# Kernel tuning notes

Hardware: AMD Instinct MI355X
Metric: run time of the kernel (lower is better)

Reference implementation:

```python
import jax, jax.numpy as jnp
import numpy as np
import math

B, T, C, H, RANK, RD = 8, 512, 2048, 16, 8, 16
HD = C // H  # 128
ADAPTER_SCALE = 1.0 / RANK  # scale / rank with scale=1.0


def setup_inputs() -> dict:
    key = jax.random.key(0)
    ks = jax.random.split(key, 7)
    x = jax.random.normal(ks[0], (B, T, C), dtype=jnp.float32)
    # frozen random linears (weights ~ N(0,1)/sqrt(in_features))
    Wqkv = jax.random.normal(ks[1], (3 * C, C), dtype=jnp.float32) / math.sqrt(C)
    Wout = jax.random.normal(ks[2], (C, C), dtype=jnp.float32) / math.sqrt(C)
    # VeRA frozen random matrices
    A0_qkv = jax.random.normal(ks[3], (RANK, C), dtype=jnp.float32) / math.sqrt(C)
    B0_qkv = jax.random.normal(ks[4], (3 * C, RANK), dtype=jnp.float32) / math.sqrt(RANK)
    A0_out = jax.random.normal(ks[5], (RANK, C), dtype=jnp.float32) / math.sqrt(C)
    B0_out = jax.random.normal(ks[6], (C, RANK), dtype=jnp.float32) / math.sqrt(RANK)
    # learned scaling vectors (init to ones, as in the module)
    d_a_qkv = jnp.ones((RANK,), dtype=jnp.float32)
    d_b_qkv = jnp.ones((RANK,), dtype=jnp.float32)
    d_a_out = jnp.ones((RANK,), dtype=jnp.float32)
    d_b_out = jnp.ones((RANK,), dtype=jnp.float32)
    # partial RoPE caches over first RD dims
    freqs = 1.0 / (10000.0 ** (jnp.arange(0, RD, 2, dtype=jnp.float32) / RD))  # [RD/2]
    ang = jnp.arange(T, dtype=jnp.float32)[:, None] * freqs[None, :]  # [T, RD/2]
    cos = jnp.cos(ang)
    sin = jnp.sin(ang)
    return {"x": x, "Wqkv": Wqkv, "A0_qkv": A0_qkv, "B0_qkv": B0_qkv,
            "d_a_qkv": d_a_qkv, "d_b_qkv": d_b_qkv,
            "Wout": Wout, "A0_out": A0_out, "B0_out": B0_out,
            "d_a_out": d_a_out, "d_b_out": d_b_out,
            "cos": cos, "sin": sin}


def _adapted_linear(x, W, A0, B0, d_a, d_b):
    # frozen(x) + VeRA adapter: diag(d_b) B0 diag(d_a) A0, scaled by 1/rank
    base = x @ W.T
    h = (x @ A0.T) * (d_a * d_b)
    return base + (h @ B0.T) * ADAPTER_SCALE


def _apply_rope(q, cos, sin):
    # q: [B, H, T, HD]; rotate first RD dims, pass-through the rest
    x_rope, x_pass = q[..., :RD], q[..., RD:]
    half = RD // 2
    x1, x2 = x_rope[..., :half], x_rope[..., half:]
    c = cos[None, None]  # [1,1,T,RD/2]
    s = sin[None, None]
    rot = jnp.concatenate([x1 * c - x2 * s, x2 * c + x1 * s], axis=-1)
    return jnp.concatenate([rot, x_pass], axis=-1)


def reference(x, Wqkv, A0_qkv, B0_qkv, d_a_qkv, d_b_qkv,
              Wout, A0_out, B0_out, d_a_out, d_b_out, cos, sin):
    qkv = _adapted_linear(x, Wqkv, A0_qkv, B0_qkv, d_a_qkv, d_b_qkv)  # [B,T,3C]
    qkv = qkv.reshape(B, T, 3, H, HD)
    q = jnp.transpose(qkv[:, :, 0], (0, 2, 1, 3))  # [B,H,T,HD]
    k = jnp.transpose(qkv[:, :, 1], (0, 2, 1, 3))
    v = jnp.transpose(qkv[:, :, 2], (0, 2, 1, 3))
    q = _apply_rope(q, cos, sin)
    k = _apply_rope(k, cos, sin)
    # causal SDPA
    scale = 1.0 / math.sqrt(HD)
    scores = jnp.einsum('bhqd,bhkd->bhqk', q, k) * scale
    mask = jnp.tril(jnp.ones((T, T), dtype=bool))
    scores = jnp.where(mask[None, None], scores, jnp.finfo(scores.dtype).min)
    attn = jax.nn.softmax(scores, axis=-1)
    y = jnp.einsum('bhqk,bhkd->bhqd', attn, v)  # [B,H,T,HD]
    y = jnp.transpose(y, (0, 2, 1, 3)).reshape(B, T, C)
    return _adapted_linear(y, Wout, A0_out, B0_out, d_a_out, d_b_out)
```

## Files before the change

kernel.cpp:

```cpp
#include <hip/hip_runtime.h>

typedef unsigned short ushort_t;
typedef __attribute__((ext_vector_type(8))) short short8;
typedef __attribute__((ext_vector_type(4))) float f32x4;

#define AS1(p) ((const __attribute__((address_space(1))) void*)(p))
#define AS3(p) ((__attribute__((address_space(3))) void*)(p))

__device__ __forceinline__ ushort_t f2bf(float f){
  unsigned u = __float_as_uint(f);
  u += 0x7FFFu + ((u>>16)&1u);
  return (ushort_t)(u>>16);
}
__device__ __forceinline__ float bf2f(ushort_t h){
  return __uint_as_float(((unsigned)h)<<16);
}

__global__ __launch_bounds__(256) void conv_f2b(const float* __restrict__ src,
                                                ushort_t* __restrict__ dst, int n){
  int i = (blockIdx.x*256 + threadIdx.x)*4;
  if (i < n){
    float4 v = *(const float4*)&src[i];
    ushort_t o0=f2bf(v.x), o1=f2bf(v.y), o2=f2bf(v.z), o3=f2bf(v.w);
    ushort4 o; o.x=o0; o.y=o1; o.z=o2; o.w=o3;
    *(ushort4*)&dst[i] = o;
  }
}

__global__ __launch_bounds__(256) void lora_h_f32(const float* __restrict__ X,
                                                  ushort_t* __restrict__ Xbf,
                                                  const float* __restrict__ A0,
                                                  const float* __restrict__ da,
                                                  const float* __restrict__ db,
                                                  float* __restrict__ out, int K){
  int m = blockIdx.x;
  int tid = threadIdx.x, lane = tid & 63, w = tid >> 6;
  float part[8] = {0,0,0,0,0,0,0,0};
  for (int k = tid; k < K; k += 256){
    float xv = X[(size_t)m*K + k];
    Xbf[(size_t)m*K + k] = f2bf(xv);
    #pragma unroll
    for (int r=0;r<8;++r) part[r] += xv * A0[r*K + k];
  }
  #pragma unroll
  for (int r=0;r<8;++r)
    for (int d=1;d<64;d<<=1) part[r] += __shfl_xor(part[r], d, 64);
  __shared__ float wsum[4][8];
  if (lane==0){
    #pragma unroll
    for (int r=0;r<8;++r) wsum[w][r] = part[r];
  }
  __syncthreads();
  if (tid < 8){
    float s = wsum[0][tid]+wsum[1][tid]+wsum[2][tid]+wsum[3][tid];
    out[(size_t)m*8 + tid] = s * da[tid]*db[tid];
  }
}

__global__ __launch_bounds__(256) void lora_h_bf16(const ushort_t* __restrict__ X,
                                                   const float* __restrict__ A0,
                                                   const float* __restrict__ da,
                                                   const float* __restrict__ db,
                                                   float* __restrict__ out, int K){
  int m = blockIdx.x;
  int tid = threadIdx.x, lane = tid & 63, w = tid >> 6;
  float part[8] = {0,0,0,0,0,0,0,0};
  for (int k = tid; k < K; k += 256){
    float xv = bf2f(X[(size_t)m*K + k]);
    #pragma unroll
    for (int r=0;r<8;++r) part[r] += xv * A0[r*K + k];
  }
  #pragma unroll
  for (int r=0;r<8;++r)
    for (int d=1;d<64;d<<=1) part[r] += __shfl_xor(part[r], d, 64);
  __shared__ float wsum[4][8];
  if (lane==0){
    #pragma unroll
    for (int r=0;r<8;++r) wsum[w][r] = part[r];
  }
  __syncthreads();
  if (tid < 8){
    float s = wsum[0][tid]+wsum[1][tid]+wsum[2][tid]+wsum[3][tid];
    out[(size_t)m*8 + tid] = s * da[tid]*db[tid];
  }
}

__global__ __launch_bounds__(512, 1) void gemm256_lora(
    const ushort_t* __restrict__ A, const ushort_t* __restrict__ Bw,
    const float* __restrict__ hmat, const float* __restrict__ B0,
    ushort_t* __restrict__ C, int M, int N, int K)
{
  __shared__ __align__(16) char smem[131072];
  const int tid = threadIdx.x, lane = tid & 63, w = tid >> 6;
  const int wm = w >> 2, wn = w & 3;

  const int nbn = N >> 8;
  const int nwg = (M >> 8) * nbn;
  const int q8 = nwg >> 3;
  const int swz = ((int)blockIdx.x & 7)*q8 + ((int)blockIdx.x >> 3);
  const int m0 = (swz / nbn) << 8, n0 = (swz % nbn) << 8;

  const int NTt = K >> 6;
  const int srow   = tid >> 3;
  const int schunk = (lane & 7) ^ (lane >> 3);

  #define STAGE_A(h, tt, bb) do { \
    const ushort_t* g_ = A + (size_t)(m0 + (h)*128 + srow)*K + (tt)*64 + schunk*8; \
    __builtin_amdgcn_global_load_lds(AS1(g_), AS3(smem + (bb)*32768 + (h)*16384 + tid*16), 16, 0, 0); \
    __builtin_amdgcn_global_load_lds(AS1(g_ + (size_t)64*K), AS3(smem + (bb)*32768 + (h)*16384 + 8192 + tid*16), 16, 0, 0); \
  } while(0)
  #define STAGE_B(h, tt, bb) do { \
    const ushort_t* g_ = Bw + (size_t)(n0 + (h)*128 + srow)*K + (tt)*64 + schunk*8; \
    __builtin_amdgcn_global_load_lds(AS1(g_), AS3(smem + 65536 + (bb)*32768 + (h)*16384 + tid*16), 16, 0, 0); \
    __builtin_amdgcn_global_load_lds(AS1(g_ + (size_t)64*K), AS3(smem + 65536 + (bb)*32768 + (h)*16384 + 8192 + tid*16), 16, 0, 0); \
  } while(0)

  #define RDA(bb, q, kk) (*(const short8*)(smem + (bb)*32768 + ((q)>>2)*16384 + \
      (((q)&3)*32 + wm*16 + (lane&15))*128 + ((((kk)*4 + (lane>>4)) ^ (lane&7))<<4)))
  #define RDB(bb, r, kk) (*(const short8*)(smem + 65536 + (bb)*32768 + ((r)>>1)*16384 + \
      (((r)&1)*64 + wn*16 + (lane&15))*128 + ((((kk)*4 + (lane>>4)) ^ (lane&7))<<4)))

  #define MM(q, ai, r, bi) do{ \
    acc[q][r] = __builtin_amdgcn_mfma_f32_16x16x32_bf16(aF[ai][0], bF[bi][0], acc[q][r], 0,0,0); \
    acc[q][r] = __builtin_amdgcn_mfma_f32_16x16x32_bf16(aF[ai][1], bF[bi][1], acc[q][r], 0,0,0); \
  }while(0)

  #define BARRIER() asm volatile("s_barrier" ::: "memory")
  #define LGKM0()  do{ asm volatile("s_waitcnt lgkmcnt(0)" ::: "memory"); __builtin_amdgcn_sched_barrier(0); }while(0)

  short8 aF[4][2];
  short8 bF[2][2];
  f32x4 acc[8][4] = {};

  STAGE_A(0,0,0); STAGE_B(0,0,0); STAGE_A(1,0,0); STAGE_B(1,0,0);
  asm volatile("s_waitcnt vmcnt(4)" ::: "memory");
  BARRIER();

  for (int t = 0; t < NTt-1; ++t){
    const int b = t & 1, nb = b ^ 1;
    #pragma unroll
    for (int q=0;q<4;++q){ aF[q][0]=RDA(b,q,0); aF[q][1]=RDA(b,q,1); }
    #pragma unroll
    for (int rl=0;rl<2;++rl){ bF[rl][0]=RDB(b,rl,0); bF[rl][1]=RDB(b,rl,1); }
    STAGE_A(0, t+1, nb);
    BARRIER(); LGKM0();
    __builtin_amdgcn_s_setprio(1);
    MM(0,0,0,0); MM(0,0,1,1); MM(1,1,0,0); MM(1,1,1,1);
    MM(2,2,0,0); MM(2,2,1,1); MM(3,3,0,0); MM(3,3,1,1);
    __builtin_amdgcn_s_setprio(0);
    asm volatile("s_waitcnt vmcnt(4)" ::: "memory");
    BARRIER();
    #pragma unroll
    for (int q=0;q<4;++q){ aF[q][0]=RDA(b,q+4,0); aF[q][1]=RDA(b,q+4,1); }
    STAGE_B(0, t+1, nb);
    BARRIER(); LGKM0();
    __builtin_amdgcn_s_setprio(1);
    MM(4,0,0,0); MM(4,0,1,1); MM(5,1,0,0); MM(5,1,1,1);
    MM(6,2,0,0); MM(6,2,1,1); MM(7,3,0,0); MM(7,3,1,1);
    __builtin_amdgcn_s_setprio(0);
    asm volatile("s_waitcnt vmcnt(4)" ::: "memory");
    BARRIER();
    #pragma unroll
    for (int q=0;q<4;++q){ aF[q][0]=RDA(b,q,0); aF[q][1]=RDA(b,q,1); }
    #pragma unroll
    for (int rl=0;rl<2;++rl){ bF[rl][0]=RDB(b,rl+2,0); bF[rl][1]=RDB(b,rl+2,1); }
    STAGE_A(1, t+1, nb);
    BARRIER(); LGKM0();
    __builtin_amdgcn_s_setprio(1);
    MM(0,0,2,0); MM(0,0,3,1); MM(1,1,2,0); MM(1,1,3,1);
    MM(2,2,2,0); MM(2,2,3,1); MM(3,3,2,0); MM(3,3,3,1);
    __builtin_amdgcn_s_setprio(0);
    BARRIER();
    #pragma unroll
    for (int q=0;q<4;++q){ aF[q][0]=RDA(b,q+4,0); aF[q][1]=RDA(b,q+4,1); }
    STAGE_B(1, t+1, nb);
    BARRIER(); LGKM0();
    __builtin_amdgcn_s_setprio(1);
    MM(4,0,2,0); MM(4,0,3,1); MM(5,1,2,0); MM(5,1,3,1);
    MM(6,2,2,0); MM(6,2,3,1); MM(7,3,2,0); MM(7,3,3,1);
    __builtin_amdgcn_s_setprio(0);
    asm volatile("s_waitcnt vmcnt(4)" ::: "memory");
    BARRIER();
  }

  {
    const int b = (NTt-1) & 1;
    #pragma unroll
    for (int q=0;q<4;++q){ aF[q][0]=RDA(b,q,0); aF[q][1]=RDA(b,q,1); }
    #pragma unroll
    for (int rl=0;rl<2;++rl){ bF[rl][0]=RDB(b,rl,0); bF[rl][1]=RDB(b,rl,1); }
    BARRIER(); LGKM0();
    __builtin_amdgcn_s_setprio(1);
    MM(0,0,0,0); MM(0,0,1,1); MM(1,1,0,0); MM(1,1,1,1);
    MM(2,2,0,0); MM(2,2,1,1); MM(3,3,0,0); MM(3,3,1,1);
    __builtin_amdgcn_s_setprio(0);
    asm volatile("s_waitcnt vmcnt(2)" ::: "memory");
    BARRIER();
    #pragma unroll
    for (int q=0;q<4;++q){ aF[q][0]=RDA(b,q+4,0); aF[q][1]=RDA(b,q+4,1); }
    BARRIER(); LGKM0();
    __builtin_amdgcn_s_setprio(1);
    MM(4,0,0,0); MM(4,0,1,1); MM(5,1,0,0); MM(5,1,1,1);
    MM(6,2,0,0); MM(6,2,1,1); MM(7,3,0,0); MM(7,3,1,1);
    __builtin_amdgcn_s_setprio(0);
    asm volatile("s_waitcnt vmcnt(0)" ::: "memory");
    BARRIER();
    #pragma unroll
    for (int q=0;q<4;++q){ aF[q][0]=RDA(b,q,0); aF[q][1]=RDA(b,q,1); }
    #pragma unroll
    for (int rl=0;rl<2;++rl){ bF[rl][0]=RDB(b,rl+2,0); bF[rl][1]=RDB(b,rl+2,1); }
    LGKM0();
    MM(0,0,2,0); MM(0,0,3,1); MM(1,1,2,0); MM(1,1,3,1);
    MM(2,2,2,0); MM(2,2,3,1); MM(3,3,2,0); MM(3,3,3,1);
    BARRIER();
    #pragma unroll
    for (int q=0;q<4;++q){ aF[q][0]=RDA(b,q+4,0); aF[q][1]=RDA(b,q+4,1); }
    LGKM0();
    MM(4,0,2,0); MM(4,0,3,1); MM(5,1,2,0); MM(5,1,3,1);
    MM(6,2,2,0); MM(6,2,3,1); MM(7,3,2,0); MM(7,3,3,1);
  }

  float b0v[4][8];
  #pragma unroll
  for (int r=0;r<4;++r){
    int col = n0 + r*64 + wn*16 + (lane&15);
    const float4* bp = (const float4*)&B0[(size_t)col*8];
    float4 u0 = bp[0], u1 = bp[1];
    b0v[r][0]=u0.x; b0v[r][1]=u0.y; b0v[r][2]=u0.z; b0v[r][3]=u0.w;
    b0v[r][4]=u1.x; b0v[r][5]=u1.y; b0v[r][6]=u1.z; b0v[r][7]=u1.w;
  }
  #pragma unroll
  for (int q=0;q<8;++q){
    #pragma unroll
    for (int jj=0;jj<4;++jj){
      int row = m0 + q*32 + wm*16 + (lane>>4)*4 + jj;
      const float4* hp = (const float4*)&hmat[(size_t)row*8];
      float4 h0 = hp[0], h1 = hp[1];
      #pragma unroll
      for (int r=0;r<4;++r){
        float lor = h0.x*b0v[r][0]+h0.y*b0v[r][1]+h0.z*b0v[r][2]+h0.w*b0v[r][3]
                  + h1.x*b0v[r][4]+h1.y*b0v[r][5]+h1.z*b0v[r][6]+h1.w*b0v[r][7];
        int col = n0 + r*64 + wn*16 + (lane&15);
        C[(size_t)row*N + col] = f2bf(acc[q][r][jj] + 0.125f*lor);
      }
    }
  }
  #undef STAGE_A
  #undef STAGE_B
  #undef RDA
  #undef RDB
  #undef MM
  #undef BARRIER
  #undef LGKM0
}

template<int MODE>
__global__ __launch_bounds__(512, 1) void gemm128x256_lora(
    const ushort_t* __restrict__ A, const ushort_t* __restrict__ Bw,
    const float* __restrict__ hmat, const float* __restrict__ B0,
    void* __restrict__ C, int M, int N, int K)
{
  __shared__ __align__(16) char smem[98304];
  const int tid = threadIdx.x, lane = tid & 63, w = tid >> 6;
  const int wm = w >> 2, wn = w & 3;

  const int nbn = N >> 8;
  const int nwg = (M >> 7) * nbn;
  const int q8 = nwg >> 3;
  const int swz = ((int)blockIdx.x & 7)*q8 + ((int)blockIdx.x >> 3);
  const int m0 = (swz / nbn) << 7, n0 = (swz % nbn) << 8;

  const int NTt = K >> 6;

  const int srow8  = tid >> 3;
  const int schunk = (lane & 7) ^ (lane >> 3);

  #define STAGE_AU(u, tt, bb) do { \
    const ushort_t* g_ = A + (size_t)(m0 + (u)*64 + srow8)*K + (tt)*64 + schunk*8; \
    __builtin_amdgcn_global_load_lds(AS1(g_), AS3(smem + (bb)*16384 + (u)*8192 + w*1024), 16, 0, 0); \
  } while(0)
  #define STAGE_BU(u, tt, bb) do { \
    const ushort_t* g_ = Bw + (size_t)(n0 + (u)*64 + srow8)*K + (tt)*64 + schunk*8; \
    __builtin_amdgcn_global_load_lds(AS1(g_), AS3(smem + 32768 + (bb)*32768 + (u)*8192 + w*1024), 16, 0, 0); \
  } while(0)

  #define RDA(bb, q, kk) (*(const short8*)(smem + (bb)*16384 + \
      ((q)*32 + wm*16 + (lane&15))*128 + ((((kk)*4 + (lane>>4)) ^ (lane&7))<<4)))
  #define RDB(bb, rg, kk) (*(const short8*)(smem + 32768 + (bb)*32768 + \
      ((rg)*64 + wn*16 + (lane&15))*128 + ((((kk)*4 + (lane>>4)) ^ (lane&7))<<4)))

  #define MM0(q,rl) do{ \
    acc[q][rl] = __builtin_amdgcn_mfma_f32_16x16x32_bf16(aF[q][0], bF[rl][0], acc[q][rl], 0,0,0); \
    acc[q][rl] = __builtin_amdgcn_mfma_f32_16x16x32_bf16(aF[q][1], bF[rl][1], acc[q][rl], 0,0,0); \
  }while(0)
  #define MM1(q,rl) do{ \
    acc[q][(rl)+2] = __builtin_amdgcn_mfma_f32_16x16x32_bf16(aF[q][0], bF[rl][0], acc[q][(rl)+2], 0,0,0); \
    acc[q][(rl)+2] = __builtin_amdgcn_mfma_f32_16x16x32_bf16(aF[q][1], bF[rl][1], acc[q][(rl)+2], 0,0,0); \
  }while(0)

  #define BARRIER() asm volatile("s_barrier" ::: "memory")

  short8 aF[4][2];
  short8 bF[2][2];
  f32x4 acc[4][4] = {};

  STAGE_AU(0,0,0); STAGE_AU(1,0,0); STAGE_BU(0,0,0); STAGE_BU(1,0,0);
  STAGE_BU(2,0,0); STAGE_BU(3,0,0);
  asm volatile("s_waitcnt vmcnt(2)" ::: "memory");
  BARRIER();

  for (int t = 0; t < NTt-1; ++t){
    const int b = t & 1, nb = b ^ 1;
    #pragma unroll
    for (int q=0;q<4;++q){ aF[q][0]=RDA(b,q,0); aF[q][1]=RDA(b,q,1); }
    #pragma unroll
    for (int rl=0;rl<2;++rl){ bF[rl][0]=RDB(b,rl,0); bF[rl][1]=RDB(b,rl,1); }
    STAGE_AU(0,t+1,nb); STAGE_AU(1,t+1,nb); STAGE_BU(0,t+1,nb); STAGE_BU(1,t+1,nb);
    __builtin_amdgcn_s_setprio(1);
    MM0(0,0); MM0(0,1); MM0(1,0); MM0(1,1);
    MM0(2,0); MM0(2,1); MM0(3,0); MM0(3,1);
    __builtin_amdgcn_s_setprio(0);
    asm volatile("s_waitcnt vmcnt(4)" ::: "memory");
    BARRIER();
    #pragma unroll
    for (int rl=0;rl<2;++rl){ bF[rl][0]=RDB(b,rl+2,0); bF[rl][1]=RDB(b,rl+2,1); }
    STAGE_BU(2,t+1,nb); STAGE_BU(3,t+1,nb);
    __builtin_amdgcn_s_setprio(1);
    MM1(0,0); MM1(0,1); MM1(1,0); MM1(1,1);
    MM1(2,0); MM1(2,1); MM1(3,0); MM1(3,1);
    __builtin_amdgcn_s_setprio(0);
    asm volatile("s_waitcnt lgkmcnt(0)" ::: "memory");
    asm volatile("s_waitcnt vmcnt(2)" ::: "memory");
    BARRIER();
  }

  {
    const int b = (NTt-1) & 1;
    #pragma unroll
    for (int q=0;q<4;++q){ aF[q][0]=RDA(b,q,0); aF[q][1]=RDA(b,q,1); }
    #pragma unroll
    for (int rl=0;rl<2;++rl){ bF[rl][0]=RDB(b,rl,0); bF[rl][1]=RDB(b,rl,1); }
    __builtin_amdgcn_s_setprio(1);
    MM0(0,0); MM0(0,1); MM0(1,0); MM0(1,1);
    MM0(2,0); MM0(2,1); MM0(3,0); MM0(3,1);
    __builtin_amdgcn_s_setprio(0);
    asm volatile("s_waitcnt vmcnt(0)" ::: "memory");
    BARRIER();
    #pragma unroll
    for (int rl=0;rl<2;++rl){ bF[rl][0]=RDB(b,rl+2,0); bF[rl][1]=RDB(b,rl+2,1); }
    MM1(0,0); MM1(0,1); MM1(1,0); MM1(1,1);
    MM1(2,0); MM1(2,1); MM1(3,0); MM1(3,1);
  }

  float b0v[4][8];
  #pragma unroll
  for (int r=0;r<4;++r){
    int col = n0 + r*64 + wn*16 + (lane&15);
    const float4* bp = (const float4*)&B0[(size_t)col*8];
    float4 u0 = bp[0], u1 = bp[1];
    b0v[r][0]=u0.x; b0v[r][1]=u0.y; b0v[r][2]=u0.z; b0v[r][3]=u0.w;
    b0v[r][4]=u1.x; b0v[r][5]=u1.y; b0v[r][6]=u1.z; b0v[r][7]=u1.w;
  }
  #pragma unroll
  for (int q=0;q<4;++q){
    #pragma unroll
    for (int jj=0;jj<4;++jj){
      int row = m0 + q*32 + wm*16 + (lane>>4)*4 + jj;
      const float4* hp = (const float4*)&hmat[(size_t)row*8];
      float4 h0 = hp[0], h1 = hp[1];
      #pragma unroll
      for (int r=0;r<4;++r){
        float lor = h0.x*b0v[r][0]+h0.y*b0v[r][1]+h0.z*b0v[r][2]+h0.w*b0v[r][3]
                  + h1.x*b0v[r][4]+h1.y*b0v[r][5]+h1.z*b0v[r][6]+h1.w*b0v[r][7];
        int col = n0 + r*64 + wn*16 + (lane&15);
        float v = acc[q][r][jj] + 0.125f*lor;
        if (MODE==0) ((ushort_t*)C)[(size_t)row*N + col] = f2bf(v);
        else         ((float*)C)[(size_t)row*N + col]    = v;
      }
    }
  }
  #undef STAGE_AU
  #undef STAGE_BU
  #undef RDA
  #undef RDB
  #undef MM0
  #undef MM1
  #undef BARRIER
}

__global__ __launch_bounds__(256) void rope_kernel(ushort_t* __restrict__ qkv,
                                                   const float* __restrict__ cosb,
                                                   const float* __restrict__ sinb){
  int idx = blockIdx.x*256 + threadIdx.x;
  int d = idx & 7;
  int g = idx >> 3;
  int h_ = g & 15;
  int s  = (g>>4) & 1;
  int t  = (g>>5) & 511;
  int b  = g >> 14;
  size_t base = (size_t)(b*512 + t)*6144 + s*2048 + h_*128;
  float x1 = bf2f(qkv[base+d]), x2 = bf2f(qkv[base+d+8]);
  float c = cosb[t*8+d], sn = sinb[t*8+d];
  qkv[base+d]   = f2bf(x1*c - x2*sn);
  qkv[base+d+8] = f2bf(x2*c + x1*sn);
}

__global__ __launch_bounds__(256) void attn_kernel(const ushort_t* __restrict__ qkv,
                                                   ushort_t* __restrict__ y){
  __shared__ __align__(16) ushort_t Ks[64*128];
  __shared__ __align__(16) ushort_t Vt[128*64];
  __shared__ __align__(16) ushort_t Pl[4][16*64];

  const int qt = blockIdx.x, hh = blockIdx.y, b = blockIdx.z;
  const int tid = threadIdx.x, lane = tid & 63, w = tid >> 6, g = lane >> 4;
  const int qb0 = qt*64;
  const int row_base = b*512;
  const int qoff = hh*128;
  const int koff = 2048 + hh*128;
  const int voff = 4096 + hh*128;
  const float scale = 0.08838834764831845f;

  short8 qf[4];
  {
    int qr = qb0 + w*16 + (lane & 15);
    const ushort_t* qp = qkv + (size_t)(row_base + qr)*6144 + qoff + g*8;
    #pragma unroll
    for (int kc=0;kc<4;++kc) qf[kc] = *(const short8*)(qp + kc*32);
  }

  const int krow = tid >> 4;
  const int kc_  = tid & 15;
  const int kcs  = (kc_ & 8) | ((kc_ ^ (krow & 7)) & 7);
  const int vr   = tid >> 2;
  const int vd0  = (tid & 3) * 32;
  const int vrhi = vr >> 3, vrlo = vr & 7;

  f32x4 o[8] = {};
  float mrow[4] = {-1e30f,-1e30f,-1e30f,-1e30f};
  float lrow[4] = {0,0,0,0};

  for (int t = 0; t <= qt; ++t){
    const int kv0 = t*64;
    __syncthreads();
    {
      const ushort_t* kg = qkv + (size_t)(row_base + kv0 + krow)*6144 + koff + kcs*8;
      #pragma unroll
      for (int i=0;i<4;++i)
        __builtin_amdgcn_global_load_lds(AS1(kg + (size_t)(i*16)*6144),
                                         AS3((char*)Ks + i*4096 + tid*16), 16, 0, 0);
    }
    {
      const ushort_t* vg = qkv + (size_t)(row_base + kv0 + vr)*6144 + voff + vd0;
      short8 vv0 = ((const short8*)vg)[0];
      short8 vv1 = ((const short8*)vg)[1];
      short8 vv2 = ((const short8*)vg)[2];
      short8 vv3 = ((const short8*)vg)[3];
      #pragma unroll
      for (int ii=0;ii<8;++ii){
        int sw = (vrhi ^ ii) << 3;
        Vt[(vd0 + ii     )*64 + sw + vrlo] = (ushort_t)vv0[ii];
        Vt[(vd0 + 8 + ii )*64 + sw + vrlo] = (ushort_t)vv1[ii];
        Vt[(vd0 + 16 + ii)*64 + sw + vrlo] = (ushort_t)vv2[ii];
        Vt[(vd0 + 24 + ii)*64 + sw + vrlo] = (ushort_t)vv3[ii];
      }
    }
    __syncthreads();

    f32x4 s4[4] = {};
    #pragma unroll
    for (int cg=0;cg<4;++cg){
      const int row = cg*16 + (lane&15);
      const int rx = row & 7;
      #pragma unroll
      for (int kc=0;kc<4;++kc){
        const int ch = kc*4 + g;
        const short8 kfv = *(const short8*)&Ks[row*128 + (((ch&8)|((ch^rx)&7))<<3)];
        s4[cg] = __builtin_amdgcn_mfma_f32_16x16x32_bf16(qf[kc], kfv, s4[cg], 0, 0, 0);
      }
    }

    const bool diag = (t == qt);
    float fac[4], p0[4], p1[4], p2[4], p3[4];
    #pragma unroll
    for (int j=0;j<4;++j){
      float a0 = s4[0][j]*scale, a1 = s4[1][j]*scale, a2 = s4[2][j]*scale, a3 = s4[3][j]*scale;
      if (diag){
        int q_abs = qb0 + w*16 + g*4 + j;
        int c0 = kv0 + (lane&15);
        if (c0      > q_abs) a0 = -1e30f;
        if (c0 + 16 > q_abs) a1 = -1e30f;
        if (c0 + 32 > q_abs) a2 = -1e30f;
        if (c0 + 48 > q_abs) a3 = -1e30f;
      }
      float mx = fmaxf(fmaxf(a0,a1), fmaxf(a2,a3));
      #pragma unroll
      for (int d=1; d<16; d<<=1) mx = fmaxf(mx, __shfl_xor(mx, d, 16));
      float mn = fmaxf(mrow[j], mx);
      float f  = __expf(mrow[j] - mn);
      mrow[j] = mn; fac[j] = f;
      p0[j] = __expf(a0 - mn); p1[j] = __expf(a1 - mn);
      p2[j] = __expf(a2 - mn); p3[j] = __expf(a3 - mn);
      float rs = p0[j] + p1[j] + p2[j] + p3[j];
      #pragma unroll
      for (int d=1; d<16; d<<=1) rs += __shfl_xor(rs, d, 16);
      lrow[j] = lrow[j]*f + rs;
    }
    #pragma unroll
    for (int n=0;n<8;++n){
      #pragma unroll
      for (int j=0;j<4;++j) o[n][j] *= fac[j];
    }

    {
      ushort_t* plw = &Pl[w][0];
      #pragma unroll
      for (int j=0;j<4;++j){
        const int prow = g*4 + j;
        const int rx = prow & 7;
        const int cl = (lane&15)>>3, c7 = lane&7;
        plw[prow*64 + (((0*2+cl)^rx)<<3) + c7] = f2bf(p0[j]);
        plw[prow*64 + (((1*2+cl)^rx)<<3) + c7] = f2bf(p1[j]);
        plw[prow*64 + (((2*2+cl)^rx)<<3) + c7] = f2bf(p2[j]);
        plw[prow*64 + (((3*2+cl)^rx)<<3) + c7] = f2bf(p3[j]);
      }
    }
    {
      const ushort_t* plw = &Pl[w][0];
      const int rowP = lane & 15, rxp = rowP & 7;
      const short8 pf0 = *(const short8*)&plw[rowP*64 + (((g  )^rxp)<<3)];
      const short8 pf1 = *(const short8*)&plw[rowP*64 + (((4+g)^rxp)<<3)];
      #pragma unroll
      for (int n=0;n<8;++n){
        const int d = n*16 + (lane&15);
        const int dx = d & 7;
        const short8 vf0 = *(const short8*)&Vt[d*64 + (((g  )^dx)<<3)];
        const short8 vf1 = *(const short8*)&Vt[d*64 + (((4+g)^dx)<<3)];
        o[n] = __builtin_amdgcn_mfma_f32_16x16x32_bf16(pf0, vf0, o[n], 0, 0, 0);
        o[n] = __builtin_amdgcn_mfma_f32_16x16x32_bf16(pf1, vf1, o[n], 0, 0, 0);
      }
    }
  }

  #pragma unroll
  for (int j=0;j<4;++j){
    float inv = 1.0f / lrow[j];
    int qr = qb0 + w*16 + g*4 + j;
    #pragma unroll
    for (int n=0;n<8;++n)
      y[(size_t)(row_base+qr)*2048 + hh*128 + n*16 + (lane&15)] = f2bf(o[n][j]*inv);
  }
}

extern "C" void kernel_launch(void* const* d_in, const int* in_sizes, int n_in,
                              void* d_out, int out_size, void* d_ws, size_t ws_size,
                              hipStream_t stream){
  const float* x       = (const float*)d_in[0];
  const float* Wqkv    = (const float*)d_in[1];
  const float* A0_qkv  = (const float*)d_in[2];
  const float* B0_qkv  = (const float*)d_in[3];
  const float* da_qkv  = (const float*)d_in[4];
  const float* db_qkv  = (const float*)d_in[5];
  const float* Wout    = (const float*)d_in[6];
  const float* A0_out  = (const float*)d_in[7];
  const float* B0_out  = (const float*)d_in[8];
  const float* da_out  = (const float*)d_in[9];
  const float* db_out  = (const float*)d_in[10];
  const float* cosb    = (const float*)d_in[11];
  const float* sinb    = (const float*)d_in[12];
  float* out = (float*)d_out;

  char* ws = (char*)d_ws;
  ushort_t* x_bf    = (ushort_t*)(ws);
  ushort_t* wqkv_bf = (ushort_t*)(ws + 16777216);
  ushort_t* wout_bf = (ushort_t*)(ws + 41943040);
  ushort_t* qkv_bf  = (ushort_t*)(ws + 50331648);
  ushort_t* y_bf    = (ushort_t*)(ws + 100663296);
  float*    h_qkv   = (float*)   (ws + 117440512);
  float*    h_out   = (float*)   (ws + 117571584);

  const int M = 4096;
  const int C = 2048;
  const int N3 = 6144;

  conv_f2b<<<12288,256, 0, stream>>>(Wqkv, wqkv_bf, N3*C);
  conv_f2b<<<4096, 256, 0, stream>>>(Wout, wout_bf, C*C);

  lora_h_f32<<<M, 256, 0, stream>>>(x, x_bf, A0_qkv, da_qkv, db_qkv, h_qkv, C);

  gemm256_lora<<<(M/256)*(N3/256), 512, 0, stream>>>(x_bf, wqkv_bf, h_qkv, B0_qkv,
                                                     qkv_bf, M, N3, C);

  rope_kernel<<<4096, 256, 0, stream>>>(qkv_bf, cosb, sinb);

  attn_kernel<<<dim3(8, 16, 8), 256, 0, stream>>>(qkv_bf, y_bf);

  lora_h_bf16<<<M, 256, 0, stream>>>(y_bf, A0_out, da_out, db_out, h_out, C);

  gemm128x256_lora<1><<<(M/128)*(C/256), 512, 0, stream>>>(y_bf, wout_bf, h_out, B0_out,
                                                           out, M, C, C);
}
```

Measured before the change: 272.5 us.

## Retile QKV GEMM to 256x192 blocks with reworked 3-phase pipeline

Changes the QKV projection GEMM tile from 256x256 to 256x192. The grid grows from 384 to 512 workgroups, which gives a whole number of waves on a 256-CU device instead of a partial second wave. The 8 waves are regrouped as 4x2, each owning a 64x96 sub-tile. The K-loop is restructured into three MFMA phases per k-step, with the next tile's loads interleaved and fewer barriers and lgkm waits. The trade-off is less operand reuse per tile and a more delicate hand-written vmcnt/barrier schedule.

New measurement: 251.5 us. 7.7% less time.

```diff
diff --git a/kernel.cpp b/kernel.cpp
--- a/kernel.cpp
+++ b/kernel.cpp
@@ -85,55 +85,53 @@
   }
 }
 
-__global__ __launch_bounds__(512, 1) void gemm256_lora(
+__global__ __launch_bounds__(512, 1) void gemm256x192_lora(
     const ushort_t* __restrict__ A, const ushort_t* __restrict__ Bw,
     const float* __restrict__ hmat, const float* __restrict__ B0,
     ushort_t* __restrict__ C, int M, int N, int K)
 {
-  __shared__ __align__(16) char smem[131072];
+  __shared__ __align__(16) char smem[114688];
   const int tid = threadIdx.x, lane = tid & 63, w = tid >> 6;
-  const int wm = w >> 2, wn = w & 3;
-
-  const int nbn = N >> 8;
+  const int wm = w >> 1, wn = w & 1;
+
+  const int nbn = N / 192;
   const int nwg = (M >> 8) * nbn;
   const int q8 = nwg >> 3;
   const int swz = ((int)blockIdx.x & 7)*q8 + ((int)blockIdx.x >> 3);
-  const int m0 = (swz / nbn) << 8, n0 = (swz % nbn) << 8;
+  const int m0 = (swz / nbn) << 8, n0 = (swz % nbn) * 192;
 
   const int NTt = K >> 6;
-  const int srow   = tid >> 3;
+  const int srow8  = tid >> 3;
   const int schunk = (lane & 7) ^ (lane >> 3);
 
-  #define STAGE_A(h, tt, bb) do { \
-    const ushort_t* g_ = A + (size_t)(m0 + (h)*128 + srow)*K + (tt)*64 + schunk*8; \
-    __builtin_amdgcn_global_load_lds(AS1(g_), AS3(smem + (bb)*32768 + (h)*16384 + tid*16), 16, 0, 0); \
-    __builtin_amdgcn_global_load_lds(AS1(g_ + (size_t)64*K), AS3(smem + (bb)*32768 + (h)*16384 + 8192 + tid*16), 16, 0, 0); \
+  #define STAGE_AU(u, tt, bb) do { \
+    const ushort_t* g_ = A + (size_t)(m0 + (u)*64 + srow8)*K + (tt)*64 + schunk*8; \
+    __builtin_amdgcn_global_load_lds(AS1(g_), AS3(smem + (bb)*32768 + (u)*8192 + tid*16), 16, 0, 0); \
   } while(0)
-  #define STAGE_B(h, tt, bb) do { \
-    const ushort_t* g_ = Bw + (size_t)(n0 + (h)*128 + srow)*K + (tt)*64 + schunk*8; \
-    __builtin_amdgcn_global_load_lds(AS1(g_), AS3(smem + 65536 + (bb)*32768 + (h)*16384 + tid*16), 16, 0, 0); \
-    __builtin_amdgcn_global_load_lds(AS1(g_ + (size_t)64*K), AS3(smem + 65536 + (bb)*32768 + (h)*16384 + 8192 + tid*16), 16, 0, 0); \
+  #define STAGE_BU(u, tt, bb) do { \
+    const ushort_t* g_ = Bw + (size_t)(n0 + (u)*64 + srow8)*K + (tt)*64 + schunk*8; \
+    __builtin_amdgcn_global_load_lds(AS1(g_), AS3(smem + 65536 + (bb)*24576 + (u)*8192 + tid*16), 16, 0, 0); \
   } while(0)
 
-  #define RDA(bb, q, kk) (*(const short8*)(smem + (bb)*32768 + ((q)>>2)*16384 + \
-      (((q)&3)*32 + wm*16 + (lane&15))*128 + ((((kk)*4 + (lane>>4)) ^ (lane&7))<<4)))
-  #define RDB(bb, r, kk) (*(const short8*)(smem + 65536 + (bb)*32768 + ((r)>>1)*16384 + \
-      (((r)&1)*64 + wn*16 + (lane&15))*128 + ((((kk)*4 + (lane>>4)) ^ (lane&7))<<4)))
-
-  #define MM(q, ai, r, bi) do{ \
-    acc[q][r] = __builtin_amdgcn_mfma_f32_16x16x32_bf16(aF[ai][0], bF[bi][0], acc[q][r], 0,0,0); \
-    acc[q][r] = __builtin_amdgcn_mfma_f32_16x16x32_bf16(aF[ai][1], bF[bi][1], acc[q][r], 0,0,0); \
+  #define RDA(bb, q, kk) (*(const short8*)(smem + (bb)*32768 + \
+      ((q)*64 + wm*16 + (lane&15))*128 + ((((kk)*4 + (lane>>4)) ^ (lane&7))<<4)))
+  #define RDB(bb, r, kk) (*(const short8*)(smem + 65536 + (bb)*24576 + \
+      ((r)*32 + wn*16 + (lane&15))*128 + ((((kk)*4 + (lane>>4)) ^ (lane&7))<<4)))
+
+  #define MM(q, r, bi) do{ \
+    acc[q][r] = __builtin_amdgcn_mfma_f32_16x16x32_bf16(aF[q][0], bF[bi][0], acc[q][r], 0,0,0); \
+    acc[q][r] = __builtin_amdgcn_mfma_f32_16x16x32_bf16(aF[q][1], bF[bi][1], acc[q][r], 0,0,0); \
   }while(0)
 
   #define BARRIER() asm volatile("s_barrier" ::: "memory")
-  #define LGKM0()  do{ asm volatile("s_waitcnt lgkmcnt(0)" ::: "memory"); __builtin_amdgcn_sched_barrier(0); }while(0)
 
   short8 aF[4][2];
   short8 bF[2][2];
-  f32x4 acc[8][4] = {};
-
-  STAGE_A(0,0,0); STAGE_B(0,0,0); STAGE_A(1,0,0); STAGE_B(1,0,0);
-  asm volatile("s_waitcnt vmcnt(4)" ::: "memory");
+  f32x4 acc[4][6] = {};
+
+  STAGE_AU(0,0,0); STAGE_AU(1,0,0); STAGE_AU(2,0,0); STAGE_AU(3,0,0);
+  STAGE_BU(0,0,0); STAGE_BU(1,0,0); STAGE_BU(2,0,0);
+  asm volatile("s_waitcnt vmcnt(2)" ::: "memory");
   BARRIER();
 
   for (int t = 0; t < NTt-1; ++t){
@@ -142,44 +140,31 @@
     for (int q=0;q<4;++q){ aF[q][0]=RDA(b,q,0); aF[q][1]=RDA(b,q,1); }
     #pragma unroll
     for (int rl=0;rl<2;++rl){ bF[rl][0]=RDB(b,rl,0); bF[rl][1]=RDB(b,rl,1); }
-    STAGE_A(0, t+1, nb);
-    BARRIER(); LGKM0();
-    __builtin_amdgcn_s_setprio(1);
-    MM(0,0,0,0); MM(0,0,1,1); MM(1,1,0,0); MM(1,1,1,1);
-    MM(2,2,0,0); MM(2,2,1,1); MM(3,3,0,0); MM(3,3,1,1);
-    __builtin_amdgcn_s_setprio(0);
-    asm volatile("s_waitcnt vmcnt(4)" ::: "memory");
-    BARRIER();
-    #pragma unroll
-    for (int q=0;q<4;++q){ aF[q][0]=RDA(b,q+4,0); aF[q][1]=RDA(b,q+4,1); }
-    STAGE_B(0, t+1, nb);
-    BARRIER(); LGKM0();
-    __builtin_amdgcn_s_setprio(1);
-    MM(4,0,0,0); MM(4,0,1,1); MM(5,1,0,0); MM(5,1,1,1);
-    MM(6,2,0,0); MM(6,2,1,1); MM(7,3,0,0); MM(7,3,1,1);
-    __builtin_amdgcn_s_setprio(0);
-    asm volatile("s_waitcnt vmcnt(4)" ::: "memory");
-    BARRIER();
-    #pragma unroll
-    for (int q=0;q<4;++q){ aF[q][0]=RDA(b,q,0); aF[q][1]=RDA(b,q,1); }
+    STAGE_AU(0,t+1,nb); STAGE_AU(1,t+1,nb);
+    __builtin_amdgcn_s_setprio(1);
+    MM(0,0,0); MM(0,1,1); MM(1,0,0); MM(1,1,1);
+    MM(2,0,0); MM(2,1,1); MM(3,0,0); MM(3,1,1);
+    __builtin_amdgcn_s_setprio(0);
+    asm volatile("s_waitcnt vmcnt(3)" ::: "memory");
+    BARRIER();
     #pragma unroll
     for (int rl=0;rl<2;++rl){ bF[rl][0]=RDB(b,rl+2,0); bF[rl][1]=RDB(b,rl+2,1); }
-    STAGE_A(1, t+1, nb);
-    BARRIER(); LGKM0();
-    __builtin_amdgcn_s_setprio(1);
-    MM(0,0,2,0); MM(0,0,3,1); MM(1,1,2,0); MM(1,1,3,1);
-    MM(2,2,2,0); MM(2,2,3,1); MM(3,3,2,0); MM(3,3,3,1);
-    __builtin_amdgcn_s_setprio(0);
-    BARRIER();
-    #pragma unroll
-    for (int q=0;q<4;++q){ aF[q][0]=RDA(b,q+4,0); aF[q][1]=RDA(b,q+4,1); }
-    STAGE_B(1, t+1, nb);
-    BARRIER(); LGKM0();
-    __builtin_amdgcn_s_setprio(1);
-    MM(4,0,2,0); MM(4,0,3,1); MM(5,1,2,0); MM(5,1,3,1);
-    MM(6,2,2,0); MM(6,2,3,1); MM(7,3,2,0); MM(7,3,3,1);
-    __builtin_amdgcn_s_setprio(0);
-    asm volatile("s_waitcnt vmcnt(4)" ::: "memory");
+    STAGE_AU(2,t+1,nb); STAGE_AU(3,t+1,nb); STAGE_BU(0,t+1,nb);
+    __builtin_amdgcn_s_setprio(1);
+    MM(0,2,0); MM(0,3,1); MM(1,2,0); MM(1,3,1);
+    MM(2,2,0); MM(2,3,1); MM(3,2,0); MM(3,3,1);
+    __builtin_amdgcn_s_setprio(0);
+    asm volatile("s_waitcnt vmcnt(5)" ::: "memory");
+    BARRIER();
+    #pragma unroll
+    for (int rl=0;rl<2;++rl){ bF[rl][0]=RDB(b,rl+4,0); bF[rl][1]=RDB(b,rl+4,1); }
+    STAGE_BU(1,t+1,nb); STAGE_BU(2,t+1,nb);
+    __builtin_amdgcn_s_setprio(1);
+    MM(0,4,0); MM(0,5,1); MM(1,4,0); MM(1,5,1);
+    MM(2,4,0); MM(2,5,1); MM(3,4,0); MM(3,5,1);
+    __builtin_amdgcn_s_setprio(0);
+    asm volatile("s_waitcnt lgkmcnt(0)" ::: "memory");
+    asm volatile("s_waitcnt vmcnt(2)" ::: "memory");
     BARRIER();
   }
 
@@ -189,69 +174,57 @@
     for (int q=0;q<4;++q){ aF[q][0]=RDA(b,q,0); aF[q][1]=RDA(b,q,1); }
     #pragma unroll
     for (int rl=0;rl<2;++rl){ bF[rl][0]=RDB(b,rl,0); bF[rl][1]=RDB(b,rl,1); }
-    BARRIER(); LGKM0();
-    __builtin_amdgcn_s_setprio(1);
-    MM(0,0,0,0); MM(0,0,1,1); MM(1,1,0,0); MM(1,1,1,1);
-    MM(2,2,0,0); MM(2,2,1,1); MM(3,3,0,0); MM(3,3,1,1);
-    __builtin_amdgcn_s_setprio(0);
-    asm volatile("s_waitcnt vmcnt(2)" ::: "memory");
-    BARRIER();
-    #pragma unroll
-    for (int q=0;q<4;++q){ aF[q][0]=RDA(b,q+4,0); aF[q][1]=RDA(b,q+4,1); }
-    BARRIER(); LGKM0();
-    __builtin_amdgcn_s_setprio(1);
-    MM(4,0,0,0); MM(4,0,1,1); MM(5,1,0,0); MM(5,1,1,1);
-    MM(6,2,0,0); MM(6,2,1,1); MM(7,3,0,0); MM(7,3,1,1);
+    __builtin_amdgcn_s_setprio(1);
+    MM(0,0,0); MM(0,1,1); MM(1,0,0); MM(1,1,1);
+    MM(2,0,0); MM(2,1,1); MM(3,0,0); MM(3,1,1);
+    __builtin_amdgcn_s_setprio(0);
+    asm volatile("s_waitcnt vmcnt(1)" ::: "memory");
+    BARRIER();
+    #pragma unroll
+    for (int rl=0;rl<2;++rl){ bF[rl][0]=RDB(b,rl+2,0); bF[rl][1]=RDB(b,rl+2,1); }
+    __builtin_amdgcn_s_setprio(1);
+    MM(0,2,0); MM(0,3,1); MM(1,2,0); MM(1,3,1);
+    MM(2,2,0); MM(2,3,1); MM(3,2,0); MM(3,3,1);
     __builtin_amdgcn_s_setprio(0);
     asm volatile("s_waitcnt vmcnt(0)" ::: "memory");
     BARRIER();
     #pragma unroll
-    for (int q=0;q<4;++q){ aF[q][0]=RDA(b,q,0); aF[q][1]=RDA(b,q,1); }
-    #pragma unroll
-    for (int rl=0;rl<2;++rl){ bF[rl][0]=RDB(b,rl+2,0); bF[rl][1]=RDB(b,rl+2,1); }
-    LGKM0();
-    MM(0,0,2,0); MM(0,0,3,1); MM(1,1,2,0); MM(1,1,3,1);
-    MM(2,2,2,0); MM(2,2,3,1); MM(3,3,2,0); MM(3,3,3,1);
-    BARRIER();
-    #pragma unroll
-    for (int q=0;q<4;++q){ aF[q][0]=RDA(b,q+4,0); aF[q][1]=RDA(b,q+4,1); }
-    LGKM0();
-    MM(4,0,2,0); MM(4,0,3,1); MM(5,1,2,0); MM(5,1,3,1);
-    MM(6,2,2,0); MM(6,2,3,1); MM(7,3,2,0); MM(7,3,3,1);
-  }
-
-  float b0v[4][8];
-  #pragma unroll
-  for (int r=0;r<4;++r){
-    int col = n0 + r*64 + wn*16 + (lane&15);
+    for (int rl=0;rl<2;++rl){ bF[rl][0]=RDB(b,rl+4,0); bF[rl][1]=RDB(b,rl+4,1); }
+    MM(0,4,0); MM(0,5,1); MM(1,4,0); MM(1,5,1);
+    MM(2,4,0); MM(2,5,1); MM(3,4,0); MM(3,5,1);
+  }
+
+  float b0v[6][8];
+  #pragma unroll
+  for (int r=0;r<6;++r){
+    int col = n0 + r*32 + wn*16 + (lane&15);
     const float4* bp = (const float4*)&B0[(size_t)col*8];
     float4 u0 = bp[0], u1 = bp[1];
     b0v[r][0]=u0.x; b0v[r][1]=u0.y; b0v[r][2]=u0.z; b0v[r][3]=u0.w;
     b0v[r][4]=u1.x; b0v[r][5]=u1.y; b0v[r][6]=u1.z; b0v[r][7]=u1.w;
   }
   #pragma unroll
-  for (int q=0;q<8;++q){
+  for (int q=0;q<4;++q){
     #pragma unroll
     for (int jj=0;jj<4;++jj){
-      int row = m0 + q*32 + wm*16 + (lane>>4)*4 + jj;
+      int row = m0 + q*64 + wm*16 + (lane>>4)*4 + jj;
       const float4* hp = (const float4*)&hmat[(size_t)row*8];
       float4 h0 = hp[0], h1 = hp[1];
       #pragma unroll
-      for (int r=0;r<4;++r){
+      for (int r=0;r<6;++r){
         float lor = h0.x*b0v[r][0]+h0.y*b0v[r][1]+h0.z*b0v[r][2]+h0.w*b0v[r][3]
                   + h1.x*b0v[r][4]+h1.y*b0v[r][5]+h1.z*b0v[r][6]+h1.w*b0v[r][7];
-        int col = n0 + r*64 + wn*16 + (lane&15);
+        int col = n0 + r*32 + wn*16 + (lane&15);
         C[(size_t)row*N + col] = f2bf(acc[q][r][jj] + 0.125f*lor);
       }
     }
   }
-  #undef STAGE_A
-  #undef STAGE_B
+  #undef STAGE_AU
+  #undef STAGE_BU
   #undef RDA
   #undef RDB
   #undef MM
   #undef BARRIER
-  #undef LGKM0
 }
 
 template<int MODE>
@@ -587,8 +560,8 @@
 
   lora_h_f32<<<M, 256, 0, stream>>>(x, x_bf, A0_qkv, da_qkv, db_qkv, h_qkv, C);
 
-  gemm256_lora<<<(M/256)*(N3/256), 512, 0, stream>>>(x_bf, wqkv_bf, h_qkv, B0_qkv,
-                                                     qkv_bf, M, N3, C);
+  gemm256x192_lora<<<(M/256)*(N3/192), 512, 0, stream>>>(x_bf, wqkv_bf, h_qkv, B0_qkv,
+                                                         qkv_bf, M, N3, C);
 
   rope_kernel<<<4096, 256, 0, stream>>>(qkv_bf, cosb, sinb);
 
```
